# Kernel tuning notes

Hardware: AMD Instinct MI355X
Metric: run time of the kernel (lower is better)

Reference implementation:

```python
import jax, jax.numpy as jnp
import numpy as np

B, N, C_IN, C_OUT, BASIS = 8, 128, 64, 64, 15
AVG_NOBJ = 49.0
NEG_SLOPE = 0.01  # torch LeakyReLU default


def eops_2_to_2_sum(x, average_nobj=AVG_NOBJ):
    """x: [B, C, N, N] -> [B, C, 15, N, N].
    5 order-zero ops + 10 sum-aggregation ops (sums normalized by average_nobj,
    double sums by average_nobj**2, as in PELICAN's 'sum' aggregation)."""
    n = x.shape[-1]
    eye = jnp.eye(n, dtype=x.dtype)                       # [N, N]
    d = jnp.diagonal(x, axis1=-2, axis2=-1)               # [B, C, N]
    rowsum = x.sum(-1) / average_nobj                      # [B, C, N]
    colsum = x.sum(-2) / average_nobj                      # [B, C, N]
    trace = d.sum(-1) / average_nobj                       # [B, C]
    allsum = x.sum((-2, -1)) / (average_nobj ** 2)         # [B, C]
    bc = lambda v: jnp.broadcast_to(v, x.shape)
    ops = [
        # --- order zero (no aggregation) ---
        d[..., :, None] * eye,                 # diag(A) embedded on diagonal
        bc(d[..., :, None]),                   # A_ii broadcast along j
        bc(d[..., None, :]),                   # A_jj broadcast along i
        x,                                     # identity
        jnp.swapaxes(x, -1, -2),               # transpose
        # --- aggregation ops ---
        rowsum[..., :, None] * eye,            # row sums on diagonal
        colsum[..., :, None] * eye,            # col sums on diagonal
        trace[..., None, None] * eye,          # trace on diagonal
        allsum[..., None, None] * eye,         # total sum on diagonal
        bc(rowsum[..., :, None]),              # rowsum_i broadcast along j
        bc(rowsum[..., None, :]),              # rowsum_j broadcast along i
        bc(colsum[..., :, None]),              # colsum_i broadcast along j
        bc(colsum[..., None, :]),              # colsum_j broadcast along i
        bc(trace[..., None, None]),            # trace broadcast everywhere
        bc(allsum[..., None, None]),           # total sum broadcast everywhere
    ]
    return jnp.stack(ops, axis=2)              # [B, C, 15, N, N]


def setup_inputs() -> dict:
    key = jax.random.key(0)
    ks = jax.random.split(key, 5)
    inputs = jax.random.normal(ks[0], (B, N, N, C_IN), jnp.float32)
    mask = jnp.ones((B, N, N, 1), jnp.float32)
    nobj = jnp.full((B,), float(N), jnp.float32)
    s_b = float(np.sqrt(1.0 / BASIS))
    s_d = float(np.sqrt(1.0 / C_IN))
    coefs00 = jax.random.normal(ks[1], (C_IN, BASIS), jnp.float32) * s_b
    coefs01 = jax.random.normal(ks[2], (C_OUT, BASIS), jnp.float32) * s_b
    coefs10 = jax.random.normal(ks[3], (C_IN, C_OUT), jnp.float32) * s_d
    coefs11 = jax.random.normal(ks[4], (C_IN, C_OUT), jnp.float32) * s_d
    bias = jnp.zeros((C_OUT,), jnp.float32)
    diag_bias = jnp.zeros((C_OUT,), jnp.float32)
    return {"inputs": inputs, "mask": mask, "nobj": nobj,
            "coefs00": coefs00, "coefs01": coefs01,
            "coefs10": coefs10, "coefs11": coefs11,
            "bias": bias, "diag_bias": diag_bias}


def reference(inputs, mask, nobj, coefs00, coefs01, coefs10, coefs11, bias, diag_bias):
    # inputs: [B, N, N, C_in] -> channels-first for basis construction
    x = jnp.transpose(inputs, (0, 3, 1, 2))                     # [B, C, N, N]
    ops = eops_2_to_2_sum(x)                                    # [B, C, 15, N, N]
    # low-rank reconstructed coefficient tensor [C_in, C_out, 15]
    coefs = (coefs00[:, None, :] * coefs10[:, :, None]
             + coefs01[None, :, :] * coefs11[:, :, None])
    out = jnp.einsum('dsb,ndbij->nijs', coefs, ops)             # [B, N, N, C_out]
    eye = jnp.eye(inputs.shape[1], dtype=out.dtype)[None, :, :, None]
    out = out + bias[None, None, None, :] + eye * diag_bias[None, None, None, :]
    out = jax.nn.leaky_relu(out, NEG_SLOPE)
    return out * mask
```

## Files before the change

### kernel.cpp

```cpp
#include <hip/hip_runtime.h>

#define BB 8
#define NN 128
#define CC 64
static constexpr float INV_A = 1.0f / 49.0f;

#define OFF_C    0
#define OFF_CB   61440
#define OFF_RS   65536
#define OFF_CS   131072
#define OFF_DV   196608
#define OFF_U1   263168
#define OFF_U2   328704
#define OFF_DG   394240

typedef __attribute__((ext_vector_type(8))) short v8s;
typedef __attribute__((ext_vector_type(4))) float v4f;

static __device__ inline unsigned pack2bf(float a, float b) {
    union { float f; unsigned u; } ua, ub; ua.f = a; ub.f = b;
    return ((ua.u + 0x8000u) >> 16) | ((ub.u + 0x8000u) & 0xffff0000u);
}
static __device__ inline unsigned short f2bf(float a) {
    union { float f; unsigned u; } ua; ua.f = a;
    return (unsigned short)((ua.u + 0x8000u) >> 16);
}

__global__ void k_pre(const float* __restrict__ in,
                      const float* __restrict__ c00, const float* __restrict__ c01,
                      const float* __restrict__ c10, const float* __restrict__ c11,
                      float* __restrict__ ws) {
    if (blockIdx.x >= 512) {
        int idx = (blockIdx.x - 512) * 256 + threadIdx.x;
        if (idx < 15 * 4096) {
            int b = idx >> 12; int r = idx & 4095; int d = r >> 6; int s = r & 63;
            ws[OFF_C + idx] = c00[d * 15 + b] * c10[d * 64 + s] + c01[s * 15 + b] * c11[d * 64 + s];
        } else if (idx < 15 * 4096 + 8192) {
            int k = idx - 15 * 4096;
            int which = k >> 12;
            int r = k & 4095; int s = r >> 6; int d = r & 63;
            int b = 3 + which;
            float v = c00[d * 15 + b] * c10[d * 64 + s] + c01[s * 15 + b] * c11[d * 64 + s];
            unsigned short* cb = (unsigned short*)(ws + OFF_CB);
            cb[s * 128 + which * 64 + d] = f2bf(v);
        }
        return;
    }
    __shared__ float4 part[4][4][16];
    int mode = blockIdx.x >> 8;
    int bb = blockIdx.x & 255;
    int n = bb >> 5; int g0 = (bb & 31) * 4;
    int t = threadIdx.x;
    int q = t >> 6; int ii = (t >> 4) & 3; int d4 = t & 15;
    float4 acc = make_float4(0.f, 0.f, 0.f, 0.f);
    if (mode == 0) {
        int i = g0 + ii;
        float4 dvv = acc; bool hd = false;
        const float* base = in + ((size_t)(n * NN + i)) * NN * CC + d4 * 4;
        for (int j = q * 32; j < q * 32 + 32; ++j) {
            float4 v = *(const float4*)(base + (size_t)j * CC);
            acc.x += v.x; acc.y += v.y; acc.z += v.z; acc.w += v.w;
            if (j == i) { dvv = v; hd = true; }
        }
        if (hd) *(float4*)(ws + OFF_DV + ((size_t)(n * NN + i)) * CC + d4 * 4) = dvv;
    } else {
        int j = g0 + ii;
        for (int i = q * 32; i < q * 32 + 32; ++i) {
            float4 v = *(const float4*)(in + (((size_t)(n * NN + i)) * NN + j) * CC + d4 * 4);
            acc.x += v.x; acc.y += v.y; acc.z += v.z; acc.w += v.w;
        }
    }
    part[q][ii][d4] = acc;
    __syncthreads();
    if (t < 64) {
        int i2 = t >> 4; int dd = t & 15;
        float4 a = part[0][i2][dd], b = part[1][i2][dd], c = part[2][i2][dd], d = part[3][i2][dd];
        float4 s;
        s.x = (a.x + b.x + c.x + d.x) * INV_A;
        s.y = (a.y + b.y + c.y + d.y) * INV_A;
        s.z = (a.z + b.z + c.z + d.z) * INV_A;
        s.w = (a.w + b.w + c.w + d.w) * INV_A;
        *(float4*)(ws + (mode ? OFF_CS : OFF_RS) + ((size_t)(n * NN + g0 + i2)) * CC + dd * 4) = s;
    }
}

__global__ __launch_bounds__(256, 4) void k_uv(const float* __restrict__ bias,
                                               const float* __restrict__ dbias,
                                               float* __restrict__ ws) {
    __shared__ float trL[64], asL[64];
    __shared__ float pU1[4][2][64], pU2[4][2][64], pDG[4][2][64];
    __shared__ float pS[4][64], pDGc[4][64];
    int n = blockIdx.x >> 6; int i0 = (blockIdx.x & 63) * 2;
    int t = threadIdx.x;
    int s = t & 63; int q = t >> 6;

    {
        float tr = 0.f, as = 0.f;
        #pragma unroll 4
        for (int e = 0; e < 32; ++e) {
            int i = q * 32 + e;
            tr += ws[OFF_DV + ((size_t)(n * NN + i)) * CC + s];
            as += ws[OFF_RS + ((size_t)(n * NN + i)) * CC + s];
        }
        pS[q][s] = tr; pDGc[q][s] = as;
        __syncthreads();
        if (t < 64) {
            trL[t] = (pS[0][t] + pS[1][t] + pS[2][t] + pS[3][t]) * INV_A;
            asL[t] = (pDGc[0][t] + pDGc[1][t] + pDGc[2][t] + pDGc[3][t]) * INV_A;
        }
        __syncthreads();
    }

    const float* C = ws + OFF_C;
    float aU1[2] = {0, 0}, aU2[2] = {0, 0}, aDG[2] = {0, 0};
    float aS = 0.f, aDGc = 0.f;
    #pragma unroll
    for (int c4 = 0; c4 < 4; ++c4) {
        int dc = q * 4 + c4;
        float tr4[4], as4[4], dv4[2][4], rs4[2][4], cs4[2][4];
        #pragma unroll
        for (int k = 0; k < 4; ++k) { tr4[k] = trL[dc * 4 + k]; as4[k] = asL[dc * 4 + k]; }
        #pragma unroll
        for (int ii = 0; ii < 2; ++ii) {
            size_t ro = ((size_t)(n * NN + i0 + ii)) * CC + dc * 4;
            float4 v = *(const float4*)(ws + OFF_DV + ro);
            dv4[ii][0] = v.x; dv4[ii][1] = v.y; dv4[ii][2] = v.z; dv4[ii][3] = v.w;
            float4 r = *(const float4*)(ws + OFF_RS + ro);
            rs4[ii][0] = r.x; rs4[ii][1] = r.y; rs4[ii][2] = r.z; rs4[ii][3] = r.w;
            float4 c = *(const float4*)(ws + OFF_CS + ro);
            cs4[ii][0] = c.x; cs4[ii][1] = c.y; cs4[ii][2] = c.z; cs4[ii][3] = c.w;
        }
        #pragma unroll
        for (int k = 0; k < 4; ++k) {
            int d = dc * 4 + k;
            const float* Cd = C + d * 64 + s;
            float c0 = Cd[0 * 4096], c1 = Cd[1 * 4096], c2 = Cd[2 * 4096];
            float c5 = Cd[5 * 4096], c6 = Cd[6 * 4096], c7 = Cd[7 * 4096];
            float c8 = Cd[8 * 4096], c9 = Cd[9 * 4096], c10v = Cd[10 * 4096];
            float c11v = Cd[11 * 4096], c12v = Cd[12 * 4096];
            float c13 = Cd[13 * 4096], c14 = Cd[14 * 4096];
            aS += c13 * tr4[k] + c14 * as4[k];
            aDGc += c7 * tr4[k] + c8 * as4[k];
            #pragma unroll
            for (int ii = 0; ii < 2; ++ii) {
                aU1[ii] += c1 * dv4[ii][k] + c9 * rs4[ii][k] + c11v * cs4[ii][k];
                aU2[ii] += c2 * dv4[ii][k] + c10v * rs4[ii][k] + c12v * cs4[ii][k];
                aDG[ii] += c0 * dv4[ii][k] + c5 * rs4[ii][k] + c6 * cs4[ii][k];
            }
        }
    }
    #pragma unroll
    for (int ii = 0; ii < 2; ++ii) {
        pU1[q][ii][s] = aU1[ii]; pU2[q][ii][s] = aU2[ii]; pDG[q][ii][s] = aDG[ii];
    }
    pS[q][s] = aS; pDGc[q][s] = aDGc;
    __syncthreads();

    if (t < 128) {
        int fi = t >> 6; int s2 = t & 63;
        float u1 = pU1[0][fi][s2] + pU1[1][fi][s2] + pU1[2][fi][s2] + pU1[3][fi][s2];
        float u2 = pU2[0][fi][s2] + pU2[1][fi][s2] + pU2[2][fi][s2] + pU2[3][fi][s2];
        float dg = pDG[0][fi][s2] + pDG[1][fi][s2] + pDG[2][fi][s2] + pDG[3][fi][s2];
        float aSt = pS[0][s2] + pS[1][s2] + pS[2][s2] + pS[3][s2];
        float aDGct = pDGc[0][s2] + pDGc[1][s2] + pDGc[2][s2] + pDGc[3][s2];
        size_t row = ((size_t)(n * NN + i0 + fi)) * CC + s2;
        ws[OFF_U1 + row] = u1 + aSt + bias[s2];
        ws[OFF_U2 + row] = u2;
        ws[OFF_DG + row] = dg + aDGct + dbias[s2];
    }
}

__global__ __launch_bounds__(256, 4) void k_main(
        const float* __restrict__ in, const float* __restrict__ mask,
        const float* __restrict__ ws, float* __restrict__ out) {
    __shared__ __align__(16) unsigned char smem[34816];
    unsigned short* Ab = (unsigned short*)smem;
    unsigned short* Bb = (unsigned short*)(smem + 17408);
    float* Obuf = (float*)smem;

    int blk = blockIdx.x;
    int n = blk >> 8; int rem = blk & 255; int i = rem >> 1; int j0 = (rem & 1) * 64;
    int t = threadIdx.x;
    int tp = t >> 4; int c = t & 15;

    const unsigned short* cb = (const unsigned short*)(ws + OFF_CB);
    #pragma unroll
    for (int e = 0; e < 4; ++e) {
        int s = e * 16 + tp;
        float4 v = *(const float4*)(cb + s * 128 + c * 8);
        *(float4*)((unsigned char*)(Bb + s * 136 + c * 8)) = v;
    }
    {
        const float* src = in + (((size_t)(n * NN + i)) * NN + j0) * CC;
        #pragma unroll
        for (int e = 0; e < 4; ++e) {
            int p = e * 16 + tp;
            float4 v = *(const float4*)(src + (size_t)p * CC + c * 4);
            uint2 pk; pk.x = pack2bf(v.x, v.y); pk.y = pack2bf(v.z, v.w);
            *(uint2*)(Ab + p * 136 + c * 4) = pk;
        }
    }
    {
        const float* srcT = in + ((size_t)(n * NN + j0) * NN + i) * CC;
        #pragma unroll
        for (int r = 0; r < 4; ++r) {
            int idx = t + r * 256;
            int p = idx >> 4; int cq = idx & 15;
            float4 v = *(const float4*)(srcT + (size_t)p * NN * CC + cq * 4);
            uint2 pk; pk.x = pack2bf(v.x, v.y); pk.y = pack2bf(v.z, v.w);
            *(uint2*)(Ab + p * 136 + 64 + cq * 4) = pk;
        }
    }
    __syncthreads();

    int w = t >> 6; int l = t & 63;
    int r16 = l & 15; int quad = l >> 4;
    v4f acc[4];
    #pragma unroll
    for (int st = 0; st < 4; ++st) acc[st] = 0.f;
    int arow = w * 16 + r16;
    #pragma unroll
    for (int kk = 0; kk < 4; ++kk) {
        v8s af = *(const v8s*)(Ab + arow * 136 + kk * 32 + quad * 8);
        #pragma unroll
        for (int st = 0; st < 4; ++st) {
            v8s bfr = *(const v8s*)(Bb + (st * 16 + r16) * 136 + kk * 32 + quad * 8);
            acc[st] = __builtin_amdgcn_mfma_f32_16x16x32_bf16(af, bfr, acc[st], 0, 0, 0);
        }
    }
    #pragma unroll
    for (int st = 0; st < 4; ++st)
        #pragma unroll
        for (int reg = 0; reg < 4; ++reg)
            Obuf[(w * 16 + quad * 4 + reg) * 68 + st * 16 + r16] = acc[st][reg];
    __syncthreads();

    int srow = (n * NN + i) * CC;
    float4 u1 = *(const float4*)(ws + OFF_U1 + srow + c * 4);
    float4 dg = *(const float4*)(ws + OFF_DG + srow + c * 4);
    #pragma unroll
    for (int e = 0; e < 4; ++e) {
        int p = e * 16 + tp;
        int j = j0 + p;
        float4 v = *(const float4*)(Obuf + p * 68 + c * 4);
        float4 u2 = *(const float4*)(ws + OFF_U2 + (n * NN + j) * CC + c * 4);
        v.x += u1.x + u2.x; v.y += u1.y + u2.y; v.z += u1.z + u2.z; v.w += u1.w + u2.w;
        if (j == i) { v.x += dg.x; v.y += dg.y; v.z += dg.z; v.w += dg.w; }
        v.x = v.x > 0.f ? v.x : 0.01f * v.x;
        v.y = v.y > 0.f ? v.y : 0.01f * v.y;
        v.z = v.z > 0.f ? v.z : 0.01f * v.z;
        v.w = v.w > 0.f ? v.w : 0.01f * v.w;
        float m = mask[((size_t)(n * NN + i)) * NN + j];
        v.x *= m; v.y *= m; v.z *= m; v.w *= m;
        *(float4*)(out + (((size_t)(n * NN + i)) * NN + j) * CC + c * 4) = v;
    }
}

extern "C" void kernel_launch(void* const* d_in, const int* in_sizes, int n_in,
                              void* d_out, int out_size, void* d_ws, size_t ws_size,
                              hipStream_t stream) {
    const float* inputs = (const float*)d_in[0];
    const float* mask   = (const float*)d_in[1];
    const float* c00 = (const float*)d_in[3];
    const float* c01 = (const float*)d_in[4];
    const float* c10 = (const float*)d_in[5];
    const float* c11 = (const float*)d_in[6];
    const float* bias  = (const float*)d_in[7];
    const float* dbias = (const float*)d_in[8];
    float* out = (float*)d_out;
    float* ws = (float*)d_ws;

    k_pre <<<784, 256, 0, stream>>>(inputs, c00, c01, c10, c11, ws);
    k_uv  <<<512, 256, 0, stream>>>(bias, dbias, ws);
    k_main<<<2048, 256, 0, stream>>>(inputs, mask, ws, out);
}
```

Before: 139.4 us.

## Process full 128-column row per block in k_main and vectorize k_uv reductions

k_main now handles all 128 j positions for a given (n,i) in one block, so each block loads the coefficient matrix into LDS once and each wave computes two 16-row MFMA tiles that share the B fragment. The grid halves to 1024 blocks, LDS grows to about 51 KB, and launch bounds drop to 3 blocks per CU. Separately, k_uv's trace and all-sum reduction uses float4 loads over 16 row groups instead of scalar strided loads. The trade-off is fewer blocks, lower occupancy and more registers per thread in exchange for less redundant staging of the coefficient matrix.

```diff
diff --git a/kernel.cpp b/kernel.cpp
--- a/kernel.cpp
+++ b/kernel.cpp
@@ -88,6 +88,7 @@
                                                const float* __restrict__ dbias,
                                                float* __restrict__ ws) {
     __shared__ float trL[64], asL[64];
+    __shared__ float4 ptr4[16][17], pas4[16][17];
     __shared__ float pU1[4][2][64], pU2[4][2][64], pDG[4][2][64];
     __shared__ float pS[4][64], pDGc[4][64];
     int n = blockIdx.x >> 6; int i0 = (blockIdx.x & 63) * 2;
@@ -95,18 +96,29 @@
     int s = t & 63; int q = t >> 6;
 
     {
-        float tr = 0.f, as = 0.f;
-        #pragma unroll 4
-        for (int e = 0; e < 32; ++e) {
-            int i = q * 32 + e;
-            tr += ws[OFF_DV + ((size_t)(n * NN + i)) * CC + s];
-            as += ws[OFF_RS + ((size_t)(n * NN + i)) * CC + s];
-        }
-        pS[q][s] = tr; pDGc[q][s] = as;
+        int d4 = t & 15; int iq = t >> 4;
+        float4 tr4 = make_float4(0.f, 0.f, 0.f, 0.f);
+        float4 as4 = tr4;
+        #pragma unroll
+        for (int e = 0; e < 8; ++e) {
+            size_t ro = ((size_t)(n * NN + iq * 8 + e)) * CC + d4 * 4;
+            float4 dv = *(const float4*)(ws + OFF_DV + ro);
+            float4 rs = *(const float4*)(ws + OFF_RS + ro);
+            tr4.x += dv.x; tr4.y += dv.y; tr4.z += dv.z; tr4.w += dv.w;
+            as4.x += rs.x; as4.y += rs.y; as4.z += rs.z; as4.w += rs.w;
+        }
+        ptr4[iq][d4] = tr4; pas4[iq][d4] = as4;
         __syncthreads();
         if (t < 64) {
-            trL[t] = (pS[0][t] + pS[1][t] + pS[2][t] + pS[3][t]) * INV_A;
-            asL[t] = (pDGc[0][t] + pDGc[1][t] + pDGc[2][t] + pDGc[3][t]) * INV_A;
+            int dd = t >> 2; int comp = t & 3;
+            float tr = 0.f, as = 0.f;
+            #pragma unroll
+            for (int g = 0; g < 16; ++g) {
+                const float* pt = (const float*)&ptr4[g][dd];
+                const float* pa = (const float*)&pas4[g][dd];
+                tr += pt[comp]; as += pa[comp];
+            }
+            trL[t] = tr * INV_A; asL[t] = as * INV_A;
         }
         __syncthreads();
     }
@@ -170,16 +182,16 @@
     }
 }
 
-__global__ __launch_bounds__(256, 4) void k_main(
+__global__ __launch_bounds__(256, 3) void k_main(
         const float* __restrict__ in, const float* __restrict__ mask,
         const float* __restrict__ ws, float* __restrict__ out) {
-    __shared__ __align__(16) unsigned char smem[34816];
+    __shared__ __align__(16) unsigned char smem[52224];
     unsigned short* Ab = (unsigned short*)smem;
-    unsigned short* Bb = (unsigned short*)(smem + 17408);
+    unsigned short* Bb = (unsigned short*)(smem + 34816);
     float* Obuf = (float*)smem;
 
     int blk = blockIdx.x;
-    int n = blk >> 8; int rem = blk & 255; int i = rem >> 1; int j0 = (rem & 1) * 64;
+    int n = blk >> 7; int i = blk & 127;
     int t = threadIdx.x;
     int tp = t >> 4; int c = t & 15;
 
@@ -191,9 +203,9 @@
         *(float4*)((unsigned char*)(Bb + s * 136 + c * 8)) = v;
     }
     {
-        const float* src = in + (((size_t)(n * NN + i)) * NN + j0) * CC;
-        #pragma unroll
-        for (int e = 0; e < 4; ++e) {
+        const float* src = in + ((size_t)(n * NN + i)) * NN * CC;
+        #pragma unroll
+        for (int e = 0; e < 8; ++e) {
             int p = e * 16 + tp;
             float4 v = *(const float4*)(src + (size_t)p * CC + c * 4);
             uint2 pk; pk.x = pack2bf(v.x, v.y); pk.y = pack2bf(v.z, v.w);
@@ -201,9 +213,9 @@
         }
     }
     {
-        const float* srcT = in + ((size_t)(n * NN + j0) * NN + i) * CC;
-        #pragma unroll
-        for (int r = 0; r < 4; ++r) {
+        const float* srcT = in + ((size_t)(n * NN) * NN + i) * CC;
+        #pragma unroll
+        for (int r = 0; r < 8; ++r) {
             int idx = t + r * 256;
             int p = idx >> 4; int cq = idx & 15;
             float4 v = *(const float4*)(srcT + (size_t)p * NN * CC + cq * 4);
@@ -215,34 +227,38 @@
 
     int w = t >> 6; int l = t & 63;
     int r16 = l & 15; int quad = l >> 4;
-    v4f acc[4];
-    #pragma unroll
-    for (int st = 0; st < 4; ++st) acc[st] = 0.f;
-    int arow = w * 16 + r16;
+    v4f acc[2][4];
+    #pragma unroll
+    for (int h = 0; h < 2; ++h)
+        #pragma unroll
+        for (int st = 0; st < 4; ++st) acc[h][st] = 0.f;
     #pragma unroll
     for (int kk = 0; kk < 4; ++kk) {
-        v8s af = *(const v8s*)(Ab + arow * 136 + kk * 32 + quad * 8);
+        v8s af0 = *(const v8s*)(Ab + (w * 32 + r16) * 136 + kk * 32 + quad * 8);
+        v8s af1 = *(const v8s*)(Ab + (w * 32 + 16 + r16) * 136 + kk * 32 + quad * 8);
         #pragma unroll
         for (int st = 0; st < 4; ++st) {
             v8s bfr = *(const v8s*)(Bb + (st * 16 + r16) * 136 + kk * 32 + quad * 8);
-            acc[st] = __builtin_amdgcn_mfma_f32_16x16x32_bf16(af, bfr, acc[st], 0, 0, 0);
-        }
-    }
-    #pragma unroll
-    for (int st = 0; st < 4; ++st)
-        #pragma unroll
-        for (int reg = 0; reg < 4; ++reg)
-            Obuf[(w * 16 + quad * 4 + reg) * 68 + st * 16 + r16] = acc[st][reg];
+            acc[0][st] = __builtin_amdgcn_mfma_f32_16x16x32_bf16(af0, bfr, acc[0][st], 0, 0, 0);
+            acc[1][st] = __builtin_amdgcn_mfma_f32_16x16x32_bf16(af1, bfr, acc[1][st], 0, 0, 0);
+        }
+    }
+    #pragma unroll
+    for (int h = 0; h < 2; ++h)
+        #pragma unroll
+        for (int st = 0; st < 4; ++st)
+            #pragma unroll
+            for (int reg = 0; reg < 4; ++reg)
+                Obuf[(w * 32 + h * 16 + quad * 4 + reg) * 68 + st * 16 + r16] = acc[h][st][reg];
     __syncthreads();
 
     int srow = (n * NN + i) * CC;
     float4 u1 = *(const float4*)(ws + OFF_U1 + srow + c * 4);
     float4 dg = *(const float4*)(ws + OFF_DG + srow + c * 4);
     #pragma unroll
-    for (int e = 0; e < 4; ++e) {
-        int p = e * 16 + tp;
-        int j = j0 + p;
-        float4 v = *(const float4*)(Obuf + p * 68 + c * 4);
+    for (int e = 0; e < 8; ++e) {
+        int j = e * 16 + tp;
+        float4 v = *(const float4*)(Obuf + j * 68 + c * 4);
         float4 u2 = *(const float4*)(ws + OFF_U2 + (n * NN + j) * CC + c * 4);
         v.x += u1.x + u2.x; v.y += u1.y + u2.y; v.z += u1.z + u2.z; v.w += u1.w + u2.w;
         if (j == i) { v.x += dg.x; v.y += dg.y; v.z += dg.z; v.w += dg.w; }
@@ -272,5 +288,5 @@
 
     k_pre <<<784, 256, 0, stream>>>(inputs, c00, c01, c10, c11, ws);
     k_uv  <<<512, 256, 0, stream>>>(bias, dbias, ws);
-    k_main<<<2048, 256, 0, stream>>>(inputs, mask, ws, out);
-}
+    k_main<<<1024, 256, 0, stream>>>(inputs, mask, ws, out);
+}
```

New measurement: 144.6 us. 1.04x slower.
